# Kernel tuning notes

Measured on AMD Instinct MI355X. Metric: run time of the kernel, lower is better.

The kernel has to match this reference:

```python
import jax, jax.numpy as jnp
import numpy as np

M, K, N = 8192, 4096, 4096
ALPHA, BETA = 0.002, 0.0005


def setup_inputs() -> dict:
    key = jax.random.key(0)
    kx, kw, kb = jax.random.split(key, 3)
    # int8-range quantized activations and weights (stored as int32 for portability)
    x = jax.random.randint(kx, (M, K), -127, 127, dtype=jnp.int32)
    weight = jax.random.randint(kw, (N, K), -127, 127, dtype=jnp.int32)  # (out, in)
    bias = jax.random.randint(kb, (1, N), -(2**20), 2**20, dtype=jnp.int32)
    alpha = jnp.float32(ALPHA)
    beta = jnp.float32(BETA)
    return {"x": x, "weight": weight, "bias": bias, "alpha": alpha, "beta": beta}


def reference(x, weight, bias, alpha, beta):
    # int8 GEMM with int32 accumulation: acc[m, n] = sum_k x[m, k] * W[n, k]
    acc = jnp.matmul(x, weight.T, preferred_element_type=jnp.int32)  # [M, N] int32
    # CUTLASS-style epilogue: D = round(alpha * acc + beta * bias) -> int32
    y = alpha * acc.astype(jnp.float32) + beta * bias.astype(jnp.float32)
    return jnp.round(y).astype(jnp.int32)
```

## Files before the change

kernel.cpp:

```cpp
#include <hip/hip_runtime.h>
#include <hip/hip_bf16.h>
#include <stdint.h>

#define M_DIM 8192
#define N_DIM 4096
#define K_DIM 4096

#define BM 256
#define BN 256
#define BK 64
#define NT (K_DIM / BK)
#define DEPTH 4

typedef int v4i __attribute__((ext_vector_type(4)));

#define AS1C(p) ((const __attribute__((address_space(1))) void*)(p))
#define AS3(p)  ((__attribute__((address_space(3))) void*)(p))

__device__ __forceinline__ int pack4(int a, int b, int c, int d) {
  return (a & 0xff) | ((b & 0xff) << 8) | ((c & 0xff) << 16) | (d << 24);
}

__global__ void pack_both_kernel(const int* __restrict__ x, const int* __restrict__ w,
                                 char* __restrict__ A8, char* __restrict__ B8,
                                 int nA, int nTot) {
  int idx = blockIdx.x * blockDim.x + threadIdx.x;
  int stride = gridDim.x * blockDim.x;
  for (int i = idx; i < nTot; i += stride) {
    const int4* pin;
    int4* pout;
    if (i < nA) {
      pin  = (const int4*)x + 4 * (size_t)i;
      pout = (int4*)A8 + i;
    } else {
      int j = i - nA;
      pin  = (const int4*)w + 4 * (size_t)j;
      pout = (int4*)B8 + j;
    }
    int4 v0 = pin[0];
    int4 v1 = pin[1];
    int4 v2 = pin[2];
    int4 v3 = pin[3];
    int4 o;
    o.x = pack4(v0.x, v0.y, v0.z, v0.w);
    o.y = pack4(v1.x, v1.y, v1.z, v1.w);
    o.z = pack4(v2.x, v2.y, v2.z, v2.w);
    o.w = pack4(v3.x, v3.y, v3.z, v3.w);
    *pout = o;
  }
}

__global__ __launch_bounds__(512, 2) void gemm_i8_kernel(
    const char* __restrict__ A8, const char* __restrict__ B8,
    const int* __restrict__ bias, const float* __restrict__ alpha_p,
    const float* __restrict__ beta_p, int* __restrict__ out) {
  __shared__ alignas(16) char lds[DEPTH][BM * BK + BN * BK];

  const int tid  = threadIdx.x;
  const int lane = tid & 63;
  const int wave = tid >> 6;

  const int orig = blockIdx.x;
  const int swz  = (orig & 7) * (512 / 8) + (orig >> 3);
  const int bm   = (swz >> 4) * BM;
  const int bn   = (swz & 15) * BN;

  int aoff[2], boff[2], ldsoff[2];
#pragma unroll
  for (int i = 0; i < 2; ++i) {
    int linear = i * 8192 + tid * 16;
    int row = linear >> 6;
    int p   = (linear >> 4) & 3;
    int g   = p ^ ((row >> 1) & 3);
    ldsoff[i] = i * 8192 + wave * 1024;
    aoff[i] = (bm + row) * K_DIM + g * 16;
    boff[i] = (bn + row) * K_DIM + g * 16;
  }

#define STAGE_A(t)                                                                  \
  do {                                                                              \
    const char* ab_ = A8 + (t) * BK;                                                \
    char* base_ = &lds[(t) & (DEPTH - 1)][0];                                       \
    _Pragma("unroll") for (int i_ = 0; i_ < 2; ++i_)                                \
      __builtin_amdgcn_global_load_lds(AS1C(ab_ + aoff[i_]),                        \
                                       AS3(base_ + ldsoff[i_]), 16, 0, 0);          \
  } while (0)

#define STAGE_B(t)                                                                  \
  do {                                                                              \
    const char* bb_ = B8 + (t) * BK;                                                \
    char* base_ = &lds[(t) & (DEPTH - 1)][0];                                       \
    _Pragma("unroll") for (int i_ = 0; i_ < 2; ++i_)                                \
      __builtin_amdgcn_global_load_lds(AS1C(bb_ + boff[i_]),                        \
                                       AS3(base_ + 16384 + ldsoff[i_]), 16, 0, 0);  \
  } while (0)

  v4i acc[8][4];
#pragma unroll
  for (int i = 0; i < 8; ++i)
#pragma unroll
    for (int j = 0; j < 4; ++j) acc[i][j] = (v4i){0, 0, 0, 0};

  const int wr = wave >> 2;
  const int wc = wave & 3;
  const int frow = lane & 15;
  const int fchunk = lane >> 4;
  const int swzoff = ((fchunk ^ ((frow >> 1) & 3)) << 4);

  STAGE_A(0); STAGE_B(0);
  STAGE_A(1); STAGE_B(1);
  STAGE_A(2); STAGE_B(2);

#define PH0(t, DO_STAGE)                                                            \
  do {                                                                              \
    if (DO_STAGE) STAGE_A((t) + 3);                                                 \
    const char* base_ = &lds[(t) & (DEPTH - 1)][0];                                 \
    _Pragma("unroll") for (int nj = 0; nj < 4; ++nj) {                              \
      int r_ = wc * 64 + nj * 16 + frow;                                            \
      bf[nj] = *(const v4i*)(base_ + 16384 + r_ * 64 + swzoff);                     \
    }                                                                               \
    v4i af_[4];                                                                     \
    _Pragma("unroll") for (int mi = 0; mi < 4; ++mi) {                              \
      int r_ = wr * 128 + mi * 16 + frow;                                           \
      af_[mi] = *(const v4i*)(base_ + r_ * 64 + swzoff);                            \
    }                                                                               \
    __builtin_amdgcn_s_setprio(1);                                                  \
    _Pragma("unroll") for (int mi = 0; mi < 4; ++mi)                                \
      _Pragma("unroll") for (int nj = 0; nj < 4; ++nj)                              \
        acc[mi][nj] = __builtin_amdgcn_mfma_i32_16x16x64_i8(af_[mi], bf[nj],        \
                                                            acc[mi][nj], 0, 0, 0); \
    __builtin_amdgcn_s_setprio(0);                                                  \
  } while (0)

#define PH1(t, DO_STAGE)                                                            \
  do {                                                                              \
    if (DO_STAGE) STAGE_B((t) + 3);                                                 \
    const char* base_ = &lds[(t) & (DEPTH - 1)][0];                                 \
    v4i af_[4];                                                                     \
    _Pragma("unroll") for (int mi = 0; mi < 4; ++mi) {                              \
      int r_ = wr * 128 + (mi + 4) * 16 + frow;                                     \
      af_[mi] = *(const v4i*)(base_ + r_ * 64 + swzoff);                            \
    }                                                                               \
    __builtin_amdgcn_s_setprio(1);                                                  \
    _Pragma("unroll") for (int mi = 0; mi < 4; ++mi)                                \
      _Pragma("unroll") for (int nj = 0; nj < 4; ++nj)                              \
        acc[mi + 4][nj] = __builtin_amdgcn_mfma_i32_16x16x64_i8(af_[mi], bf[nj],    \
                                                            acc[mi + 4][nj],       \
                                                            0, 0, 0);              \
    __builtin_amdgcn_s_setprio(0);                                                  \
  } while (0)

  for (int t = 0; t < NT - 2; ++t) {
    v4i bf[4];
    asm volatile("s_waitcnt vmcnt(8) lgkmcnt(0)" ::: "memory");
    __builtin_amdgcn_s_barrier();
    PH0(t, t + 3 < NT);
    __builtin_amdgcn_s_barrier();
    PH1(t, t + 3 < NT);
  }
  {
    v4i bf[4];
    asm volatile("s_waitcnt vmcnt(4) lgkmcnt(0)" ::: "memory");
    __builtin_amdgcn_s_barrier();
    PH0(NT - 2, false);
    __builtin_amdgcn_s_barrier();
    PH1(NT - 2, false);
  }
  {
    v4i bf[4];
    asm volatile("s_waitcnt vmcnt(0) lgkmcnt(0)" ::: "memory");
    __builtin_amdgcn_s_barrier();
    PH0(NT - 1, false);
    __builtin_amdgcn_s_barrier();
    PH1(NT - 1, false);
  }

  const float alpha = *alpha_p;
  const float beta  = *beta_p;
  const int col0 = bn + wc * 64 + frow;
  float bb4[4];
#pragma unroll
  for (int nj = 0; nj < 4; ++nj) bb4[nj] = beta * (float)bias[col0 + nj * 16];

  const int rbase = bm + wr * 128 + (lane >> 4) * 4;
#pragma unroll
  for (int mi = 0; mi < 8; ++mi) {
#pragma unroll
    for (int r = 0; r < 4; ++r) {
      size_t rowoff = (size_t)(rbase + mi * 16 + r) * N_DIM;
#pragma unroll
      for (int nj = 0; nj < 4; ++nj) {
        out[rowoff + col0 + nj * 16] =
            (int)rintf(fmaf(alpha, (float)acc[mi][nj][r], bb4[nj]));
      }
    }
  }
#undef STAGE_A
#undef STAGE_B
#undef PH0
#undef PH1
}

__global__ void naive_kernel(const int* __restrict__ x, const int* __restrict__ w,
                             const int* __restrict__ bias,
                             const float* __restrict__ alpha_p,
                             const float* __restrict__ beta_p,
                             int* __restrict__ out) {
  size_t idx = (size_t)blockIdx.x * 256 + threadIdx.x;
  int m = (int)(idx / N_DIM);
  int n = (int)(idx % N_DIM);
  const int4* xr = (const int4*)(x + (size_t)m * K_DIM);
  const int4* wr = (const int4*)(w + (size_t)n * K_DIM);
  int acc = 0;
  for (int k = 0; k < K_DIM / 4; ++k) {
    int4 a = xr[k];
    int4 b = wr[k];
    acc += a.x * b.x + a.y * b.y + a.z * b.z + a.w * b.w;
  }
  out[idx] = (int)rintf(fmaf(*alpha_p, (float)acc, (*beta_p) * (float)bias[n]));
}

extern "C" void kernel_launch(void* const* d_in, const int* in_sizes, int n_in,
                              void* d_out, int out_size, void* d_ws, size_t ws_size,
                              hipStream_t stream) {
  const int*   x     = (const int*)d_in[0];
  const int*   w     = (const int*)d_in[1];
  const int*   bias  = (const int*)d_in[2];
  const float* alpha = (const float*)d_in[3];
  const float* beta  = (const float*)d_in[4];
  int* out = (int*)d_out;

  const size_t a8_bytes = (size_t)M_DIM * K_DIM;
  const size_t b8_bytes = (size_t)N_DIM * K_DIM;

  if (ws_size >= a8_bytes + b8_bytes) {
    char* A8 = (char*)d_ws;
    char* B8 = A8 + a8_bytes;
    const int nA = (int)(a8_bytes / 16);
    const int nTot = (int)((a8_bytes + b8_bytes) / 16);
    pack_both_kernel<<<2048, 256, 0, stream>>>(x, w, A8, B8, nA, nTot);
    const int nblk = (M_DIM / BM) * (N_DIM / BN);
    gemm_i8_kernel<<<nblk, 512, 0, stream>>>(A8, B8, bias, alpha, beta, out);
  } else {
    naive_kernel<<<(M_DIM * (size_t)N_DIM) / 256, 256, 0, stream>>>(x, w, bias, alpha, beta, out);
  }
}
```

Baseline: 183.6 us.

## Software-pipeline LDS fragment reads with register double-buffering and one barrier per tile

The int8 GEMM main loop is restructured so the next K-tile's low A and B fragments are read from LDS into a second register set while the current tile's MFMAs run. The loop is unrolled by two and uses a single barrier per tile instead of two. A and B global-to-LDS staging is merged into one issue point, and sched_barriers pin the read/MFMA interleaving. The aim is to hide LDS read latency and cut synchronization stalls, at the cost of more live vector registers, which may reduce occupancy or cause spills.

New measurement: 183.8 us. No clear change (+0.1%).

```diff
diff --git a/kernel.cpp b/kernel.cpp
--- a/kernel.cpp
+++ b/kernel.cpp
@@ -77,22 +77,17 @@
     boff[i] = (bn + row) * K_DIM + g * 16;
   }
 
-#define STAGE_A(t)                                                                  \
+#define STAGE_AB(t)                                                                 \
   do {                                                                              \
     const char* ab_ = A8 + (t) * BK;                                                \
+    const char* bb_ = B8 + (t) * BK;                                                \
     char* base_ = &lds[(t) & (DEPTH - 1)][0];                                       \
-    _Pragma("unroll") for (int i_ = 0; i_ < 2; ++i_)                                \
+    _Pragma("unroll") for (int i_ = 0; i_ < 2; ++i_) {                              \
       __builtin_amdgcn_global_load_lds(AS1C(ab_ + aoff[i_]),                        \
                                        AS3(base_ + ldsoff[i_]), 16, 0, 0);          \
-  } while (0)
-
-#define STAGE_B(t)                                                                  \
-  do {                                                                              \
-    const char* bb_ = B8 + (t) * BK;                                                \
-    char* base_ = &lds[(t) & (DEPTH - 1)][0];                                       \
-    _Pragma("unroll") for (int i_ = 0; i_ < 2; ++i_)                                \
       __builtin_amdgcn_global_load_lds(AS1C(bb_ + boff[i_]),                        \
                                        AS3(base_ + 16384 + ldsoff[i_]), 16, 0, 0);  \
+    }                                                                               \
   } while (0)
 
   v4i acc[8][4];
@@ -107,73 +102,84 @@
   const int fchunk = lane >> 4;
   const int swzoff = ((fchunk ^ ((frow >> 1) & 3)) << 4);
 
-  STAGE_A(0); STAGE_B(0);
-  STAGE_A(1); STAGE_B(1);
-  STAGE_A(2); STAGE_B(2);
-
-#define PH0(t, DO_STAGE)                                                            \
-  do {                                                                              \
-    if (DO_STAGE) STAGE_A((t) + 3);                                                 \
+  v4i bf0[4], aflo0[4], bf1[4], aflo1[4], afhi[4];
+
+#define READ_LO(S, t)                                                               \
+  do {                                                                              \
     const char* base_ = &lds[(t) & (DEPTH - 1)][0];                                 \
-    _Pragma("unroll") for (int nj = 0; nj < 4; ++nj) {                              \
-      int r_ = wc * 64 + nj * 16 + frow;                                            \
-      bf[nj] = *(const v4i*)(base_ + 16384 + r_ * 64 + swzoff);                     \
-    }                                                                               \
-    v4i af_[4];                                                                     \
-    _Pragma("unroll") for (int mi = 0; mi < 4; ++mi) {                              \
-      int r_ = wr * 128 + mi * 16 + frow;                                           \
-      af_[mi] = *(const v4i*)(base_ + r_ * 64 + swzoff);                            \
-    }                                                                               \
+    _Pragma("unroll") for (int nj = 0; nj < 4; ++nj)                                \
+      bf##S[nj] = *(const v4i*)(base_ + 16384 + (wc * 64 + nj * 16 + frow) * 64 +   \
+                                swzoff);                                            \
+    _Pragma("unroll") for (int mi = 0; mi < 4; ++mi)                                \
+      aflo##S[mi] = *(const v4i*)(base_ + (wr * 128 + mi * 16 + frow) * 64 +        \
+                                  swzoff);                                          \
+  } while (0)
+
+#define READ_HI(t)                                                                  \
+  do {                                                                              \
+    const char* base_ = &lds[(t) & (DEPTH - 1)][0];                                 \
+    _Pragma("unroll") for (int mi = 0; mi < 4; ++mi)                                \
+      afhi[mi] = *(const v4i*)(base_ + (wr * 128 + (mi + 4) * 16 + frow) * 64 +     \
+                               swzoff);                                             \
+  } while (0)
+
+#define MFMA_LO(S)                                                                  \
+  do {                                                                              \
     __builtin_amdgcn_s_setprio(1);                                                  \
     _Pragma("unroll") for (int mi = 0; mi < 4; ++mi)                                \
       _Pragma("unroll") for (int nj = 0; nj < 4; ++nj)                              \
-        acc[mi][nj] = __builtin_amdgcn_mfma_i32_16x16x64_i8(af_[mi], bf[nj],        \
+        acc[mi][nj] = __builtin_amdgcn_mfma_i32_16x16x64_i8(aflo##S[mi], bf##S[nj], \
                                                             acc[mi][nj], 0, 0, 0); \
     __builtin_amdgcn_s_setprio(0);                                                  \
   } while (0)
 
-#define PH1(t, DO_STAGE)                                                            \
-  do {                                                                              \
-    if (DO_STAGE) STAGE_B((t) + 3);                                                 \
-    const char* base_ = &lds[(t) & (DEPTH - 1)][0];                                 \
-    v4i af_[4];                                                                     \
-    _Pragma("unroll") for (int mi = 0; mi < 4; ++mi) {                              \
-      int r_ = wr * 128 + (mi + 4) * 16 + frow;                                     \
-      af_[mi] = *(const v4i*)(base_ + r_ * 64 + swzoff);                            \
-    }                                                                               \
+#define MFMA_HI(S)                                                                  \
+  do {                                                                              \
     __builtin_amdgcn_s_setprio(1);                                                  \
     _Pragma("unroll") for (int mi = 0; mi < 4; ++mi)                                \
       _Pragma("unroll") for (int nj = 0; nj < 4; ++nj)                              \
-        acc[mi + 4][nj] = __builtin_amdgcn_mfma_i32_16x16x64_i8(af_[mi], bf[nj],    \
-                                                            acc[mi + 4][nj],       \
-                                                            0, 0, 0);              \
+        acc[mi + 4][nj] = __builtin_amdgcn_mfma_i32_16x16x64_i8(afhi[mi], bf##S[nj],\
+                                                                acc[mi + 4][nj],   \
+                                                                0, 0, 0);          \
     __builtin_amdgcn_s_setprio(0);                                                  \
   } while (0)
 
-  for (int t = 0; t < NT - 2; ++t) {
-    v4i bf[4];
-    asm volatile("s_waitcnt vmcnt(8) lgkmcnt(0)" ::: "memory");
-    __builtin_amdgcn_s_barrier();
-    PH0(t, t + 3 < NT);
-    __builtin_amdgcn_s_barrier();
-    PH1(t, t + 3 < NT);
-  }
-  {
-    v4i bf[4];
-    asm volatile("s_waitcnt vmcnt(4) lgkmcnt(0)" ::: "memory");
-    __builtin_amdgcn_s_barrier();
-    PH0(NT - 2, false);
-    __builtin_amdgcn_s_barrier();
-    PH1(NT - 2, false);
-  }
-  {
-    v4i bf[4];
-    asm volatile("s_waitcnt vmcnt(0) lgkmcnt(0)" ::: "memory");
-    __builtin_amdgcn_s_barrier();
-    PH0(NT - 1, false);
-    __builtin_amdgcn_s_barrier();
-    PH1(NT - 1, false);
-  }
+#define ITER(t, C, N, DO_STAGE)                                                     \
+  do {                                                                              \
+    asm volatile("s_waitcnt vmcnt(4) lgkmcnt(0)" ::: "memory");                     \
+    __builtin_amdgcn_s_barrier();                                                   \
+    if (DO_STAGE) STAGE_AB((t) + 3);                                                \
+    READ_HI(t);                                                                     \
+    __builtin_amdgcn_sched_barrier(0);                                              \
+    MFMA_LO(C);                                                                     \
+    READ_LO(N, (t) + 1);                                                            \
+    __builtin_amdgcn_sched_barrier(0);                                              \
+    MFMA_HI(C);                                                                     \
+  } while (0)
+
+  STAGE_AB(0);
+  STAGE_AB(1);
+  STAGE_AB(2);
+  asm volatile("s_waitcnt vmcnt(8)" ::: "memory");
+  __builtin_amdgcn_s_barrier();
+  READ_LO(0, 0);
+
+  for (int t = 0; t < NT - 2; t += 2) {
+    ITER(t, 0, 1, true);
+    ITER(t + 1, 1, 0, (t + 4) < NT);
+  }
+  asm volatile("s_waitcnt vmcnt(0) lgkmcnt(0)" ::: "memory");
+  __builtin_amdgcn_s_barrier();
+  READ_HI(NT - 2);
+  __builtin_amdgcn_sched_barrier(0);
+  MFMA_LO(0);
+  READ_LO(1, NT - 1);
+  __builtin_amdgcn_sched_barrier(0);
+  MFMA_HI(0);
+  READ_HI(NT - 1);
+  __builtin_amdgcn_sched_barrier(0);
+  MFMA_LO(1);
+  MFMA_HI(1);
 
   const float alpha = *alpha_p;
   const float beta  = *beta_p;
@@ -195,10 +201,12 @@
       }
     }
   }
-#undef STAGE_A
-#undef STAGE_B
-#undef PH0
-#undef PH1
+#undef STAGE_AB
+#undef READ_LO
+#undef READ_HI
+#undef MFMA_LO
+#undef MFMA_HI
+#undef ITER
 }
 
 __global__ void naive_kernel(const int* __restrict__ x, const int* __restrict__ w,
```

## Reschedule int8 GEMM main loop to issue LDS reads before global prefetch and barriers

Applied to the files above, without the earlier changes.

Restructures the K-loop into read/stage/barrier/MFMA phases. Each phase issues its LDS fragment reads first, then the next tile's global-to-LDS prefetch, then a barrier and an lgkmcnt wait before the MFMA block. The global-memory wait moves to the end of each iteration, and the tail iterations are peeled to match. The aim is to overlap LDS read latency and prefetch issue with other waves' MFMA work, in a ping-pong style. In exchange, the extra A/B fragment registers (aflo/afhi) raise register pressure, and the barrier placement becomes more delicate.

After: 187.9 us. 2.4% more time.

```diff
diff --git a/kernel.cpp b/kernel.cpp
--- a/kernel.cpp
+++ b/kernel.cpp
@@ -107,73 +107,88 @@
   const int fchunk = lane >> 4;
   const int swzoff = ((fchunk ^ ((frow >> 1) & 3)) << 4);
 
+  v4i bf[4], aflo[4], afhi[4];
+
+#define READ0(t)                                                                    \
+  do {                                                                              \
+    const char* base_ = &lds[(t) & (DEPTH - 1)][0];                                 \
+    _Pragma("unroll") for (int nj = 0; nj < 4; ++nj)                                \
+      bf[nj] = *(const v4i*)(base_ + 16384 + (wc * 64 + nj * 16 + frow) * 64 +      \
+                             swzoff);                                               \
+    _Pragma("unroll") for (int mi = 0; mi < 4; ++mi)                                \
+      aflo[mi] = *(const v4i*)(base_ + (wr * 128 + mi * 16 + frow) * 64 + swzoff);  \
+  } while (0)
+
+#define READ1(t)                                                                    \
+  do {                                                                              \
+    const char* base_ = &lds[(t) & (DEPTH - 1)][0];                                 \
+    _Pragma("unroll") for (int mi = 0; mi < 4; ++mi)                                \
+      afhi[mi] = *(const v4i*)(base_ + (wr * 128 + (mi + 4) * 16 + frow) * 64 +     \
+                               swzoff);                                             \
+  } while (0)
+
+#define MFMA_LO()                                                                   \
+  do {                                                                              \
+    __builtin_amdgcn_s_setprio(1);                                                  \
+    _Pragma("unroll") for (int mi = 0; mi < 4; ++mi)                                \
+      _Pragma("unroll") for (int nj = 0; nj < 4; ++nj)                              \
+        acc[mi][nj] = __builtin_amdgcn_mfma_i32_16x16x64_i8(aflo[mi], bf[nj],       \
+                                                            acc[mi][nj], 0, 0, 0); \
+    __builtin_amdgcn_s_setprio(0);                                                  \
+  } while (0)
+
+#define MFMA_HI()                                                                   \
+  do {                                                                              \
+    __builtin_amdgcn_s_setprio(1);                                                  \
+    _Pragma("unroll") for (int mi = 0; mi < 4; ++mi)                                \
+      _Pragma("unroll") for (int nj = 0; nj < 4; ++nj)                              \
+        acc[mi + 4][nj] = __builtin_amdgcn_mfma_i32_16x16x64_i8(afhi[mi], bf[nj],   \
+                                                                acc[mi + 4][nj],   \
+                                                                0, 0, 0);          \
+    __builtin_amdgcn_s_setprio(0);                                                  \
+  } while (0)
+
+#define PHASE0(t, DO_STAGE)                                                         \
+  do {                                                                              \
+    READ0(t);                                                                       \
+    if (DO_STAGE) STAGE_A((t) + 3);                                                 \
+    __builtin_amdgcn_s_barrier();                                                   \
+    asm volatile("s_waitcnt lgkmcnt(0)" ::: "memory");                              \
+    MFMA_LO();                                                                      \
+    __builtin_amdgcn_s_barrier();                                                   \
+  } while (0)
+
+#define PHASE1(t, DO_STAGE)                                                         \
+  do {                                                                              \
+    READ1(t);                                                                       \
+    if (DO_STAGE) STAGE_B((t) + 3);                                                 \
+    __builtin_amdgcn_s_barrier();                                                   \
+    asm volatile("s_waitcnt lgkmcnt(0)" ::: "memory");                              \
+    MFMA_HI();                                                                      \
+  } while (0)
+
   STAGE_A(0); STAGE_B(0);
   STAGE_A(1); STAGE_B(1);
   STAGE_A(2); STAGE_B(2);
-
-#define PH0(t, DO_STAGE)                                                            \
-  do {                                                                              \
-    if (DO_STAGE) STAGE_A((t) + 3);                                                 \
-    const char* base_ = &lds[(t) & (DEPTH - 1)][0];                                 \
-    _Pragma("unroll") for (int nj = 0; nj < 4; ++nj) {                              \
-      int r_ = wc * 64 + nj * 16 + frow;                                            \
-      bf[nj] = *(const v4i*)(base_ + 16384 + r_ * 64 + swzoff);                     \
-    }                                                                               \
-    v4i af_[4];                                                                     \
-    _Pragma("unroll") for (int mi = 0; mi < 4; ++mi) {                              \
-      int r_ = wr * 128 + mi * 16 + frow;                                           \
-      af_[mi] = *(const v4i*)(base_ + r_ * 64 + swzoff);                            \
-    }                                                                               \
-    __builtin_amdgcn_s_setprio(1);                                                  \
-    _Pragma("unroll") for (int mi = 0; mi < 4; ++mi)                                \
-      _Pragma("unroll") for (int nj = 0; nj < 4; ++nj)                              \
-        acc[mi][nj] = __builtin_amdgcn_mfma_i32_16x16x64_i8(af_[mi], bf[nj],        \
-                                                            acc[mi][nj], 0, 0, 0); \
-    __builtin_amdgcn_s_setprio(0);                                                  \
-  } while (0)
-
-#define PH1(t, DO_STAGE)                                                            \
-  do {                                                                              \
-    if (DO_STAGE) STAGE_B((t) + 3);                                                 \
-    const char* base_ = &lds[(t) & (DEPTH - 1)][0];                                 \
-    v4i af_[4];                                                                     \
-    _Pragma("unroll") for (int mi = 0; mi < 4; ++mi) {                              \
-      int r_ = wr * 128 + (mi + 4) * 16 + frow;                                     \
-      af_[mi] = *(const v4i*)(base_ + r_ * 64 + swzoff);                            \
-    }                                                                               \
-    __builtin_amdgcn_s_setprio(1);                                                  \
-    _Pragma("unroll") for (int mi = 0; mi < 4; ++mi)                                \
-      _Pragma("unroll") for (int nj = 0; nj < 4; ++nj)                              \
-        acc[mi + 4][nj] = __builtin_amdgcn_mfma_i32_16x16x64_i8(af_[mi], bf[nj],    \
-                                                            acc[mi + 4][nj],       \
-                                                            0, 0, 0);              \
-    __builtin_amdgcn_s_setprio(0);                                                  \
-  } while (0)
-
-  for (int t = 0; t < NT - 2; ++t) {
-    v4i bf[4];
-    asm volatile("s_waitcnt vmcnt(8) lgkmcnt(0)" ::: "memory");
+  asm volatile("s_waitcnt vmcnt(8)" ::: "memory");
+  __builtin_amdgcn_s_barrier();
+
+  for (int t = 0; t < NT - 3; ++t) {
+    PHASE0(t, true);
+    PHASE1(t, true);
+    asm volatile("s_waitcnt vmcnt(8)" ::: "memory");
     __builtin_amdgcn_s_barrier();
-    PH0(t, t + 3 < NT);
-    __builtin_amdgcn_s_barrier();
-    PH1(t, t + 3 < NT);
-  }
-  {
-    v4i bf[4];
-    asm volatile("s_waitcnt vmcnt(4) lgkmcnt(0)" ::: "memory");
-    __builtin_amdgcn_s_barrier();
-    PH0(NT - 2, false);
-    __builtin_amdgcn_s_barrier();
-    PH1(NT - 2, false);
-  }
-  {
-    v4i bf[4];
-    asm volatile("s_waitcnt vmcnt(0) lgkmcnt(0)" ::: "memory");
-    __builtin_amdgcn_s_barrier();
-    PH0(NT - 1, false);
-    __builtin_amdgcn_s_barrier();
-    PH1(NT - 1, false);
-  }
+  }
+  PHASE0(NT - 3, false);
+  PHASE1(NT - 3, false);
+  asm volatile("s_waitcnt vmcnt(4)" ::: "memory");
+  __builtin_amdgcn_s_barrier();
+  PHASE0(NT - 2, false);
+  PHASE1(NT - 2, false);
+  asm volatile("s_waitcnt vmcnt(0)" ::: "memory");
+  __builtin_amdgcn_s_barrier();
+  PHASE0(NT - 1, false);
+  PHASE1(NT - 1, false);
 
   const float alpha = *alpha_p;
   const float beta  = *beta_p;
@@ -197,8 +212,12 @@
   }
 #undef STAGE_A
 #undef STAGE_B
-#undef PH0
-#undef PH1
+#undef READ0
+#undef READ1
+#undef MFMA_LO
+#undef MFMA_HI
+#undef PHASE0
+#undef PHASE1
 }
 
 __global__ void naive_kernel(const int* __restrict__ x, const int* __restrict__ w,
```
